# Kernel tuning notes

Measured on AMD Instinct MI355X. Metric: run time of the kernel, lower is better.

The kernel has to match this reference:

```python
import jax, jax.numpy as jnp
import numpy as np

N = 1024
X_DIM = 128
Y_DIM = 128
HID = 256


def setup_inputs() -> dict:
    key = jax.random.key(0)
    ks = jax.random.split(key, 8)
    x_samples = jax.random.normal(ks[0], (N, X_DIM), dtype=jnp.float32)
    y_samples = jax.random.normal(ks[1], (N, Y_DIM), dtype=jnp.float32)
    # F_func: Linear(x_dim+y_dim -> hidden), ReLU, Linear(hidden -> 1)
    W1 = jax.random.normal(ks[2], (HID, X_DIM + Y_DIM), dtype=jnp.float32) * 0.05
    b1 = jax.random.normal(ks[3], (HID,), dtype=jnp.float32) * 0.05
    w2 = jax.random.normal(ks[4], (HID,), dtype=jnp.float32) * 0.05  # Linear(hidden,1) weight
    b2 = jax.random.normal(ks[5], (), dtype=jnp.float32) * 0.05
    # baseline: Linear(y_dim -> 1)
    wb = jax.random.normal(ks[6], (Y_DIM,), dtype=jnp.float32) * 0.05
    bb = jax.random.normal(ks[7], (), dtype=jnp.float32) * 0.05
    return {"x_samples": x_samples, "y_samples": y_samples,
            "W1": W1, "b1": b1, "w2": w2, "b2": b2, "wb": wb, "bb": bb}


def reference(x_samples, y_samples, W1, b1, w2, b2, wb, bb):
    n = y_samples.shape[0]
    # Split first linear: F(x,y) first layer = x @ Wx^T + y @ Wy^T + b1
    # (identical math to Linear on concat([x, y]))
    Wx = W1[:, :X_DIM]  # [H, x_dim]
    Wy = W1[:, X_DIM:]  # [H, y_dim]
    px = x_samples @ Wx.T  # [N, H]
    py = y_samples @ Wy.T  # [N, H]

    # T0: F on paired samples (x_i, y_i) -> [N]
    T0 = jax.nn.relu(px + py + b1) @ w2 + b2

    # T1[i, j] = F(x_j, y_i): x tiled over dim 0, y tiled over dim 1
    h = jax.nn.relu(px[None, :, :] + py[:, None, :] + b1)  # [N, N, H]
    T1 = h @ w2 + b2  # [N, N]

    # baseline log-scores on y -> [N]
    log_scores = y_samples @ wb + bb

    # (T1 - log_scores) broadcasts log_scores along dim 1 (the j/x axis),
    # matching torch's [N,N,1] - [N,1] broadcast; logsumexp over dim 1.
    lse = jax.scipy.special.logsumexp(T1 - log_scores[None, :], axis=1)  # [N]
    log_n = jnp.log(jnp.asarray(n, dtype=T1.dtype))
    lower_bound = (1.0 + T0.mean() - log_scores.mean()
                   - jnp.exp(lse - log_n).mean())
    return lower_bound
```

## Files before the change

kernel.cpp:

```cpp
#include <hip/hip_runtime.h>
#include <hip/hip_fp16.h>

#define NN 1024
#define HID 256
#define XD 128

typedef _Float16 h2 __attribute__((ext_vector_type(2)));
typedef _Float16 h8 __attribute__((ext_vector_type(8)));

#define WSF_BYTE_OFF 1049600
#define F_C    0
#define F_PART 1024
#define F_T0P  5120
#define F_LSP  5376

__device__ __forceinline__ h2 relu2(h2 x) {
  h2 z = {(_Float16)0, (_Float16)0};
  return __builtin_elementwise_max(x, z);
}

__device__ __forceinline__ float dot2f(h2 a, h2 b, float c) {
  return __builtin_amdgcn_fdot2(a, b, c, false);
}

__global__ __launch_bounds__(256) void prep_kernel(
    const float* __restrict__ x, const float* __restrict__ y,
    const float* __restrict__ W1, const float* __restrict__ b1,
    const float* __restrict__ w2, const float* __restrict__ b2p,
    const float* __restrict__ wb, const float* __restrict__ bbp,
    _Float16* __restrict__ wsh, float* __restrict__ wsf)
{
  __shared__ float sx[4][128];
  __shared__ float sy[4][128];
  __shared__ float st0[4][4];
  __shared__ float sls[4];
  const int t = threadIdx.x;
  const int blk = blockIdx.x;
  const int r0 = blk * 4;

  {
    const int rl = (t & 127) >> 5, f = t & 31;
    if (t < 128) {
      *(float4*)&sx[rl][f * 4] = *(const float4*)(x + (r0 + rl) * XD + f * 4);
    } else {
      *(float4*)&sy[rl][f * 4] = *(const float4*)(y + (r0 + rl) * XD + f * 4);
    }
  }
  __syncthreads();

  const int k = t;
  float apx[4] = {0,0,0,0};
  float apy[4] = {0,0,0,0};
  const float* wrow = W1 + k * 256;
  for (int dq = 0; dq < 32; ++dq) {
    float4 wx = *(const float4*)(wrow + dq * 4);
    float4 wy = *(const float4*)(wrow + 128 + dq * 4);
#pragma unroll
    for (int r = 0; r < 4; ++r) {
      float4 xv = *(const float4*)&sx[r][dq * 4];
      float4 yv = *(const float4*)&sy[r][dq * 4];
      apx[r] = fmaf(xv.x, wx.x, apx[r]);
      apx[r] = fmaf(xv.y, wx.y, apx[r]);
      apx[r] = fmaf(xv.z, wx.z, apx[r]);
      apx[r] = fmaf(xv.w, wx.w, apx[r]);
      apy[r] = fmaf(yv.x, wy.x, apy[r]);
      apy[r] = fmaf(yv.y, wy.y, apy[r]);
      apy[r] = fmaf(yv.z, wy.z, apy[r]);
      apy[r] = fmaf(yv.w, wy.w, apy[r]);
    }
  }
  const float b1k = b1[k];
#pragma unroll
  for (int r = 0; r < 4; ++r) apy[r] += b1k;

  {
    _Float16* pxh = wsh;
    _Float16* pyh = wsh + 262144;
    const int kg = k >> 5, ks = (k >> 3) & 3, kl = k & 7;
#pragma unroll
    for (int r = 0; r < 4; ++r) {
      const int j = r0 + r;
      const int jt = j >> 7, jj = (j >> 6) & 1, ln = j & 63;
      pxh[((jt * 8 + kg) * 8 + ks * 2 + jj) * 512 + ln * 8 + kl]
          = (_Float16)apx[r];
      pyh[j * 256 + k] = (_Float16)apy[r];
    }
  }

  const float w2k = w2[k];
  const float b2v = b2p[0];
  const int wv = t >> 6, lane = t & 63;
#pragma unroll
  for (int r = 0; r < 4; ++r) {
    float v = fmaxf(apx[r] + apy[r], 0.f) * w2k;
    for (int o = 32; o > 0; o >>= 1) v += __shfl_down(v, o);
    if (lane == 0) st0[wv][r] = v;
  }

  if (t < 128) {
    const int rl = t >> 5, f = t & 31;
    float p = 0.f;
#pragma unroll
    for (int l = 0; l < 4; ++l) p = fmaf(sy[rl][f * 4 + l], wb[f * 4 + l], p);
    for (int m = 16; m > 0; m >>= 1) p += __shfl_xor(p, m);
    if (f == 0) {
      const float lsv = p + bbp[0];
      sls[rl] = lsv;
      wsf[F_C + r0 + rl] = __expf(b2v - lsv);
    }
  }
  __syncthreads();
  if (t == 0) {
    float t0s = 0.f, lss = 0.f;
#pragma unroll
    for (int r = 0; r < 4; ++r) {
      t0s += st0[0][r] + st0[1][r] + st0[2][r] + st0[3][r] + b2v;
      lss += sls[r];
    }
    wsf[F_T0P + blk] = t0s;
    wsf[F_LSP + blk] = lss;
  }
  if (blk == 0 && t < 128) {
    h2 wv2;
    wv2.x = (_Float16)w2[2 * t];
    wv2.y = (_Float16)w2[2 * t + 1];
    ((h2*)(wsh + 524288))[t] = wv2;
  }
}

__global__ __launch_bounds__(512) void main_kernel(
    const _Float16* __restrict__ wsh, float* __restrict__ wsf)
{
  __shared__ _Float16 spy[16 * 256];
  __shared__ _Float16 sw2[256];
  __shared__ float sComb[4][16][128];
  const int t = threadIdx.x;
  const int lane = t & 63;
  const int kg = t >> 6;
  const int blk = blockIdx.x;
  const int bj = blk & 7;
  const int i0 = (blk >> 3) * 16;

  h8 pxr[8];
  {
    const float4* gpx = (const float4*)wsh + ((bj * 8 + kg) * 8) * 64 + lane;
#pragma unroll
    for (int q = 0; q < 8; ++q) ((float4*)pxr)[q] = gpx[q * 64];
  }
  {
    const float4* gpy = (const float4*)(wsh + 262144 + (size_t)i0 * 256);
    ((float4*)spy)[t] = gpy[t];
    if (t < 32) ((float4*)sw2)[t] = ((const float4*)(wsh + 524288))[t];
  }
  __syncthreads();

  h8 w2r[4];
#pragma unroll
  for (int q = 0; q < 4; ++q) w2r[q] = ((const h8*)(sw2 + kg * 32))[q];

  float acc[16][2];
#pragma unroll
  for (int ii = 0; ii < 16; ++ii) { acc[ii][0] = 0.f; acc[ii][1] = 0.f; }

#pragma unroll
  for (int ii = 0; ii < 16; ++ii) {
    const h8* prow = (const h8*)(spy + ii * 256 + kg * 32);
#pragma unroll
    for (int ks = 0; ks < 4; ++ks) {
      h8 pv = prow[ks];
      const h2* p2 = (const h2*)&pv;
      const h2* wp = (const h2*)&w2r[ks];
#pragma unroll
      for (int jj = 0; jj < 2; ++jj) {
        const h2* x2 = (const h2*)&pxr[ks * 2 + jj];
        float s = acc[ii][jj];
        s = dot2f(relu2(x2[0] + p2[0]), wp[0], s);
        s = dot2f(relu2(x2[1] + p2[1]), wp[1], s);
        s = dot2f(relu2(x2[2] + p2[2]), wp[2], s);
        s = dot2f(relu2(x2[3] + p2[3]), wp[3], s);
        acc[ii][jj] = s;
      }
    }
  }

  if (kg >= 4) {
#pragma unroll
    for (int ii = 0; ii < 16; ++ii) {
      sComb[kg - 4][ii][lane]      = acc[ii][0];
      sComb[kg - 4][ii][lane + 64] = acc[ii][1];
    }
  }
  __syncthreads();
  if (kg < 4) {
#pragma unroll
    for (int ii = 0; ii < 16; ++ii) {
      acc[ii][0] += sComb[kg][ii][lane];
      acc[ii][1] += sComb[kg][ii][lane + 64];
    }
  }
  __syncthreads();
  if (kg == 2 || kg == 3) {
#pragma unroll
    for (int ii = 0; ii < 16; ++ii) {
      sComb[kg - 2][ii][lane]      = acc[ii][0];
      sComb[kg - 2][ii][lane + 64] = acc[ii][1];
    }
  }
  __syncthreads();
  if (kg < 2) {
#pragma unroll
    for (int ii = 0; ii < 16; ++ii) {
      acc[ii][0] += sComb[kg][ii][lane];
      acc[ii][1] += sComb[kg][ii][lane + 64];
    }
  }
  __syncthreads();
  if (kg == 1) {
#pragma unroll
    for (int ii = 0; ii < 16; ++ii) {
      sComb[0][ii][lane]      = acc[ii][0];
      sComb[0][ii][lane + 64] = acc[ii][1];
    }
  }
  __syncthreads();
  if (kg == 0) {
    const float* cbase = wsf + F_C + bj * 128;
    const float c0 = cbase[lane], c1 = cbase[64 + lane];
    float ts = 0.f;
#pragma unroll
    for (int ii = 0; ii < 16; ++ii) {
      ts += __expf(acc[ii][0] + sComb[0][ii][lane]) * c0;
      ts += __expf(acc[ii][1] + sComb[0][ii][lane + 64]) * c1;
    }
    for (int o = 32; o > 0; o >>= 1) ts += __shfl_down(ts, o);
    if (lane == 0) wsf[F_PART + blk] = ts;
  }
}

__global__ __launch_bounds__(256) void fin_kernel(
    const float* __restrict__ wsf, float* __restrict__ out)
{
  __shared__ float sr[4][3];
  const int t = threadIdx.x;
  float e = 0.f;
  if (t < 128) {
    float4 ev = ((const float4*)(wsf + F_PART))[t];
    e = (ev.x + ev.y) + (ev.z + ev.w);
  }
  float t0 = wsf[F_T0P + t];
  float ls = wsf[F_LSP + t];
  for (int o = 32; o > 0; o >>= 1) {
    e  += __shfl_down(e, o);
    t0 += __shfl_down(t0, o);
    ls += __shfl_down(ls, o);
  }
  if ((t & 63) == 0) {
    sr[t >> 6][0] = e;
    sr[t >> 6][1] = t0;
    sr[t >> 6][2] = ls;
  }
  __syncthreads();
  if (t == 0) {
    const float es  = sr[0][0] + sr[1][0] + sr[2][0] + sr[3][0];
    const float t0s = sr[0][1] + sr[1][1] + sr[2][1] + sr[3][1];
    const float lss = sr[0][2] + sr[1][2] + sr[2][2] + sr[3][2];
    out[0] = 1.0f + t0s * (1.0f / 1024.0f) - lss * (1.0f / 1024.0f)
                  - es * (1.0f / 1048576.0f);
  }
}

extern "C" void kernel_launch(void* const* d_in, const int* in_sizes, int n_in,
                              void* d_out, int out_size, void* d_ws, size_t ws_size,
                              hipStream_t stream) {
  const float* x  = (const float*)d_in[0];
  const float* y  = (const float*)d_in[1];
  const float* W1 = (const float*)d_in[2];
  const float* b1 = (const float*)d_in[3];
  const float* w2 = (const float*)d_in[4];
  const float* b2 = (const float*)d_in[5];
  const float* wb = (const float*)d_in[6];
  const float* bb = (const float*)d_in[7];
  _Float16* wsh = (_Float16*)d_ws;
  float* wsf = (float*)((char*)d_ws + WSF_BYTE_OFF);
  float* out = (float*)d_out;

  hipLaunchKernelGGL(prep_kernel, dim3(256), dim3(256), 0, stream,
                     x, y, W1, b1, w2, b2, wb, bb, wsh, wsf);
  hipLaunchKernelGGL(main_kernel, dim3(512), dim3(512), 0, stream, wsh, wsf);
  hipLaunchKernelGGL(fin_kernel, dim3(1), dim3(256), 0, stream, wsf, out);
}
```

Baseline: 35.68 us.

## Split hidden dim across blocks, write partial T1, add combine kernel

Retiles the main kernel so each block handles half the hidden dimension (kh) for 8 i-rows by 256 j-columns, doubling the grid to 1024 blocks with a launch-bounds occupancy hint. The px layout in prep is reorganised to match. Each half writes full fp32 partial T1 tiles (two 4 MB buffers) to workspace, and a new combine kernel sums the halves and applies exp and the per-column weights before reduction. This gives more parallelism and lower register pressure per block, at the cost of about 8 MB of extra global writes and reads plus one more kernel launch.

```diff
diff --git a/kernel.cpp b/kernel.cpp
--- a/kernel.cpp
+++ b/kernel.cpp
@@ -9,10 +9,12 @@
 typedef _Float16 h8 __attribute__((ext_vector_type(8)));
 
 #define WSF_BYTE_OFF 1049600
-#define F_C    0
-#define F_PART 1024
-#define F_T0P  5120
-#define F_LSP  5376
+#define F_C     0
+#define F_T0P   1024
+#define F_LSP   1280
+#define F_PART  1536
+#define F_PA    4096
+#define F_PB    1052672
 
 __device__ __forceinline__ h2 relu2(h2 x) {
   h2 z = {(_Float16)0, (_Float16)0};
@@ -76,12 +78,12 @@
   {
     _Float16* pxh = wsh;
     _Float16* pyh = wsh + 262144;
-    const int kg = k >> 5, ks = (k >> 3) & 3, kl = k & 7;
+    const int kh = k >> 7, kg = (k >> 4) & 7, ks = (k >> 3) & 1, kl = k & 7;
 #pragma unroll
     for (int r = 0; r < 4; ++r) {
       const int j = r0 + r;
-      const int jt = j >> 7, jj = (j >> 6) & 1, ln = j & 63;
-      pxh[((jt * 8 + kg) * 8 + ks * 2 + jj) * 512 + ln * 8 + kl]
+      const int jt = j >> 8, jj = (j >> 6) & 3, ln = j & 63;
+      pxh[(((((jt * 2 + kh) * 8 + kg) * 4 + jj) * 2 + ks) * 64 + ln) * 8 + kl]
           = (_Float16)apx[r];
       pyh[j * 256 + k] = (_Float16)apy[r];
     }
@@ -128,113 +130,149 @@
   }
 }
 
-__global__ __launch_bounds__(512) void main_kernel(
+__global__ __launch_bounds__(512, 4) void main_kernel(
     const _Float16* __restrict__ wsh, float* __restrict__ wsf)
 {
-  __shared__ _Float16 spy[16 * 256];
-  __shared__ _Float16 sw2[256];
-  __shared__ float sComb[4][16][128];
+  __shared__ _Float16 spy[8 * 128];
+  __shared__ _Float16 sw2[128];
+  __shared__ float sComb[4][8][256];
   const int t = threadIdx.x;
   const int lane = t & 63;
   const int kg = t >> 6;
   const int blk = blockIdx.x;
-  const int bj = blk & 7;
-  const int i0 = (blk >> 3) * 16;
-
-  h8 pxr[8];
+  const int kh = blk & 1;
+  const int ig = (blk >> 1) & 127;
+  const int jt = blk >> 8;
+
+  if (t < 128) {
+    const int row = t >> 4, col = t & 15;
+    ((float4*)spy)[t] =
+        ((const float4*)(wsh + 262144))[(ig * 8 + row) * 32 + kh * 16 + col];
+  } else if (t < 144) {
+    ((float4*)sw2)[t - 128] = ((const float4*)(wsh + 524288))[kh * 16 + (t - 128)];
+  }
+
+  h8 pxA[4], pxB[4];
   {
-    const float4* gpx = (const float4*)wsh + ((bj * 8 + kg) * 8) * 64 + lane;
-#pragma unroll
-    for (int q = 0; q < 8; ++q) ((float4*)pxr)[q] = gpx[q * 64];
-  }
-  {
-    const float4* gpy = (const float4*)(wsh + 262144 + (size_t)i0 * 256);
-    ((float4*)spy)[t] = gpy[t];
-    if (t < 32) ((float4*)sw2)[t] = ((const float4*)(wsh + 524288))[t];
-  }
-  __syncthreads();
-
-  h8 w2r[4];
-#pragma unroll
-  for (int q = 0; q < 4; ++q) w2r[q] = ((const h8*)(sw2 + kg * 32))[q];
-
-  float acc[16][2];
-#pragma unroll
-  for (int ii = 0; ii < 16; ++ii) { acc[ii][0] = 0.f; acc[ii][1] = 0.f; }
-
-#pragma unroll
-  for (int ii = 0; ii < 16; ++ii) {
-    const h8* prow = (const h8*)(spy + ii * 256 + kg * 32);
-#pragma unroll
-    for (int ks = 0; ks < 4; ++ks) {
-      h8 pv = prow[ks];
-      const h2* p2 = (const h2*)&pv;
-      const h2* wp = (const h2*)&w2r[ks];
-#pragma unroll
-      for (int jj = 0; jj < 2; ++jj) {
-        const h2* x2 = (const h2*)&pxr[ks * 2 + jj];
-        float s = acc[ii][jj];
-        s = dot2f(relu2(x2[0] + p2[0]), wp[0], s);
-        s = dot2f(relu2(x2[1] + p2[1]), wp[1], s);
-        s = dot2f(relu2(x2[2] + p2[2]), wp[2], s);
-        s = dot2f(relu2(x2[3] + p2[3]), wp[3], s);
-        acc[ii][jj] = s;
-      }
+    const float4* gpx = (const float4*)wsh;
+    const int pbase = (((jt * 2 + kh) * 8 + kg) * 4) * 2 * 64 + lane;
+#pragma unroll
+    for (int jj = 0; jj < 4; ++jj) {
+      *(float4*)&pxA[jj] = gpx[pbase + (jj * 2 + 0) * 64];
+      *(float4*)&pxB[jj] = gpx[pbase + (jj * 2 + 1) * 64];
+    }
+  }
+  __syncthreads();
+
+  const h8* wf = (const h8*)(sw2 + kg * 16);
+  h8 w0 = wf[0], w1 = wf[1];
+  const h2* wA = (const h2*)&w0;
+  const h2* wB = (const h2*)&w1;
+
+  float acc[8][4];
+#pragma unroll
+  for (int ii = 0; ii < 8; ++ii)
+#pragma unroll
+    for (int jj = 0; jj < 4; ++jj) acc[ii][jj] = 0.f;
+
+#pragma unroll
+  for (int ii = 0; ii < 8; ++ii) {
+    const h8* pf = (const h8*)(spy + ii * 128 + kg * 16);
+    h8 p0 = pf[0], p1 = pf[1];
+    const h2* pA = (const h2*)&p0;
+    const h2* pB = (const h2*)&p1;
+#pragma unroll
+    for (int jj = 0; jj < 4; ++jj) {
+      const h2* xA = (const h2*)&pxA[jj];
+      const h2* xB = (const h2*)&pxB[jj];
+      float s = acc[ii][jj];
+      s = dot2f(relu2(xA[0] + pA[0]), wA[0], s);
+      s = dot2f(relu2(xA[1] + pA[1]), wA[1], s);
+      s = dot2f(relu2(xA[2] + pA[2]), wA[2], s);
+      s = dot2f(relu2(xA[3] + pA[3]), wA[3], s);
+      s = dot2f(relu2(xB[0] + pB[0]), wB[0], s);
+      s = dot2f(relu2(xB[1] + pB[1]), wB[1], s);
+      s = dot2f(relu2(xB[2] + pB[2]), wB[2], s);
+      s = dot2f(relu2(xB[3] + pB[3]), wB[3], s);
+      acc[ii][jj] = s;
     }
   }
 
   if (kg >= 4) {
 #pragma unroll
-    for (int ii = 0; ii < 16; ++ii) {
-      sComb[kg - 4][ii][lane]      = acc[ii][0];
-      sComb[kg - 4][ii][lane + 64] = acc[ii][1];
-    }
+    for (int ii = 0; ii < 8; ++ii)
+#pragma unroll
+      for (int jj = 0; jj < 4; ++jj)
+        sComb[kg - 4][ii][jj * 64 + lane] = acc[ii][jj];
   }
   __syncthreads();
   if (kg < 4) {
 #pragma unroll
-    for (int ii = 0; ii < 16; ++ii) {
-      acc[ii][0] += sComb[kg][ii][lane];
-      acc[ii][1] += sComb[kg][ii][lane + 64];
-    }
+    for (int ii = 0; ii < 8; ++ii)
+#pragma unroll
+      for (int jj = 0; jj < 4; ++jj)
+        acc[ii][jj] += sComb[kg][ii][jj * 64 + lane];
   }
   __syncthreads();
   if (kg == 2 || kg == 3) {
 #pragma unroll
-    for (int ii = 0; ii < 16; ++ii) {
-      sComb[kg - 2][ii][lane]      = acc[ii][0];
-      sComb[kg - 2][ii][lane + 64] = acc[ii][1];
-    }
+    for (int ii = 0; ii < 8; ++ii)
+#pragma unroll
+      for (int jj = 0; jj < 4; ++jj)
+        sComb[kg - 2][ii][jj * 64 + lane] = acc[ii][jj];
   }
   __syncthreads();
   if (kg < 2) {
 #pragma unroll
-    for (int ii = 0; ii < 16; ++ii) {
-      acc[ii][0] += sComb[kg][ii][lane];
-      acc[ii][1] += sComb[kg][ii][lane + 64];
-    }
+    for (int ii = 0; ii < 8; ++ii)
+#pragma unroll
+      for (int jj = 0; jj < 4; ++jj)
+        acc[ii][jj] += sComb[kg][ii][jj * 64 + lane];
   }
   __syncthreads();
   if (kg == 1) {
 #pragma unroll
-    for (int ii = 0; ii < 16; ++ii) {
-      sComb[0][ii][lane]      = acc[ii][0];
-      sComb[0][ii][lane + 64] = acc[ii][1];
-    }
+    for (int ii = 0; ii < 8; ++ii)
+#pragma unroll
+      for (int jj = 0; jj < 4; ++jj)
+        sComb[0][ii][jj * 64 + lane] = acc[ii][jj];
   }
   __syncthreads();
   if (kg == 0) {
-    const float* cbase = wsf + F_C + bj * 128;
-    const float c0 = cbase[lane], c1 = cbase[64 + lane];
-    float ts = 0.f;
-#pragma unroll
-    for (int ii = 0; ii < 16; ++ii) {
-      ts += __expf(acc[ii][0] + sComb[0][ii][lane]) * c0;
-      ts += __expf(acc[ii][1] + sComb[0][ii][lane + 64]) * c1;
-    }
-    for (int o = 32; o > 0; o >>= 1) ts += __shfl_down(ts, o);
-    if (lane == 0) wsf[F_PART + blk] = ts;
-  }
+    float* pout = wsf + (kh ? F_PB : F_PA) + (size_t)((jt * 128 + ig) * 8) * 256;
+#pragma unroll
+    for (int ii = 0; ii < 8; ++ii)
+#pragma unroll
+      for (int jj = 0; jj < 4; ++jj)
+        pout[ii * 256 + jj * 64 + lane] =
+            acc[ii][jj] + sComb[0][ii][jj * 64 + lane];
+  }
+}
+
+__global__ __launch_bounds__(256) void combine_kernel(
+    const float* __restrict__ wsf, float* __restrict__ wsfo)
+{
+  __shared__ float sred[4];
+  const int t = threadIdx.x;
+  const int blk = blockIdx.x;
+  const float4* pA4 = (const float4*)(wsf + F_PA);
+  const float4* pB4 = (const float4*)(wsf + F_PB);
+  float ts = 0.f;
+#pragma unroll
+  for (int r = 0; r < 4; ++r) {
+    const int idx4 = blk * 1024 + r * 256 + t;
+    float4 a = pA4[idx4];
+    float4 b = pB4[idx4];
+    const int jt = idx4 >> 16;
+    float4 c4 = ((const float4*)(wsf + F_C + jt * 256))[idx4 & 63];
+    ts += __expf(a.x + b.x) * c4.x + __expf(a.y + b.y) * c4.y
+        + __expf(a.z + b.z) * c4.z + __expf(a.w + b.w) * c4.w;
+  }
+  for (int o = 32; o > 0; o >>= 1) ts += __shfl_down(ts, o);
+  if ((t & 63) == 0) sred[t >> 6] = ts;
+  __syncthreads();
+  if (t == 0)
+    wsfo[F_PART + blk] = (sred[0] + sred[1]) + (sred[2] + sred[3]);
 }
 
 __global__ __launch_bounds__(256) void fin_kernel(
@@ -242,11 +280,7 @@
 {
   __shared__ float sr[4][3];
   const int t = threadIdx.x;
-  float e = 0.f;
-  if (t < 128) {
-    float4 ev = ((const float4*)(wsf + F_PART))[t];
-    e = (ev.x + ev.y) + (ev.z + ev.w);
-  }
+  float e  = wsf[F_PART + t];
   float t0 = wsf[F_T0P + t];
   float ls = wsf[F_LSP + t];
   for (int o = 32; o > 0; o >>= 1) {
@@ -286,6 +320,7 @@
 
   hipLaunchKernelGGL(prep_kernel, dim3(256), dim3(256), 0, stream,
                      x, y, W1, b1, w2, b2, wb, bb, wsh, wsf);
-  hipLaunchKernelGGL(main_kernel, dim3(512), dim3(512), 0, stream, wsh, wsf);
+  hipLaunchKernelGGL(main_kernel, dim3(1024), dim3(512), 0, stream, wsh, wsf);
+  hipLaunchKernelGGL(combine_kernel, dim3(256), dim3(256), 0, stream, wsf, wsf);
   hipLaunchKernelGGL(fin_kernel, dim3(1), dim3(256), 0, stream, wsf, out);
 }
```

Measured after the change: 39.69 us. 1.11x slower.

## Fuse prep, main and final kernels into one cooperative kernel with grid syncs

Applied to the files above, without the earlier changes.

Merges the three launches into a single cooperative kernel of 256 blocks × 512 threads, separated by grid-wide syncs, to remove per-launch overhead and inter-kernel gaps. The prep phase now splits the x and y projections across the two halves of the block. The main phase has each block handle two 16-row i-tiles in a loop, so 256 blocks cover the former 512-block grid. The trade-offs are the cost of grid barriers, fewer blocks in the main phase (half the previous parallelism), and a dependence on all blocks being co-resident.

```diff
diff --git a/kernel.cpp b/kernel.cpp
--- a/kernel.cpp
+++ b/kernel.cpp
@@ -1,5 +1,6 @@
 #include <hip/hip_runtime.h>
 #include <hip/hip_fp16.h>
+#include <hip/hip_cooperative_groups.h>
 
 #define NN 1024
 #define HID 256
@@ -9,10 +10,10 @@
 typedef _Float16 h8 __attribute__((ext_vector_type(8)));
 
 #define WSF_BYTE_OFF 1049600
-#define F_C    0
-#define F_PART 1024
-#define F_T0P  5120
-#define F_LSP  5376
+#define F_C     0
+#define F_T0P   1024
+#define F_LSP   1280
+#define F_PART  1536
 
 __device__ __forceinline__ h2 relu2(h2 x) {
   h2 z = {(_Float16)0, (_Float16)0};
@@ -23,249 +24,281 @@
   return __builtin_amdgcn_fdot2(a, b, c, false);
 }
 
-__global__ __launch_bounds__(256) void prep_kernel(
+__global__ __launch_bounds__(512) void fused_kernel(
     const float* __restrict__ x, const float* __restrict__ y,
     const float* __restrict__ W1, const float* __restrict__ b1,
     const float* __restrict__ w2, const float* __restrict__ b2p,
     const float* __restrict__ wb, const float* __restrict__ bbp,
-    _Float16* __restrict__ wsh, float* __restrict__ wsf)
+    _Float16* __restrict__ wsh, float* __restrict__ wsf,
+    float* __restrict__ out)
 {
-  __shared__ float sx[4][128];
-  __shared__ float sy[4][128];
-  __shared__ float st0[4][4];
-  __shared__ float sls[4];
+  __shared__ __align__(16) char smem[41024];
   const int t = threadIdx.x;
   const int blk = blockIdx.x;
-  const int r0 = blk * 4;
 
   {
-    const int rl = (t & 127) >> 5, f = t & 31;
+    float* sx   = (float*)smem;
+    float* sy   = sx + 512;
+    float* spy2 = sy + 512;
+    float* st0  = spy2 + 1024;
+    float* sls  = st0 + 16;
+    const int r0 = blk * 4;
+
     if (t < 128) {
-      *(float4*)&sx[rl][f * 4] = *(const float4*)(x + (r0 + rl) * XD + f * 4);
+      const int rl = t >> 5, f = t & 31;
+      *(float4*)(sx + rl * 128 + f * 4) = *(const float4*)(x + (r0 + rl) * XD + f * 4);
+    } else if (t < 256) {
+      const int t2 = t - 128, rl = t2 >> 5, f = t2 & 31;
+      *(float4*)(sy + rl * 128 + f * 4) = *(const float4*)(y + (r0 + rl) * XD + f * 4);
+    }
+    __syncthreads();
+
+    const int side = t >> 8;
+    const int k = t & 255;
+    float ap[4] = {0.f, 0.f, 0.f, 0.f};
+    const float* wrow = W1 + k * 256 + side * 128;
+    const float* sm0 = side ? sy : sx;
+#pragma unroll 8
+    for (int dq = 0; dq < 32; ++dq) {
+      float4 wv = *(const float4*)(wrow + dq * 4);
+#pragma unroll
+      for (int r = 0; r < 4; ++r) {
+        float4 sv = *(const float4*)(sm0 + r * 128 + dq * 4);
+        ap[r] = fmaf(sv.x, wv.x, ap[r]);
+        ap[r] = fmaf(sv.y, wv.y, ap[r]);
+        ap[r] = fmaf(sv.z, wv.z, ap[r]);
+        ap[r] = fmaf(sv.w, wv.w, ap[r]);
+      }
+    }
+
+    if (side == 1) {
+      const float b1k = b1[k];
+#pragma unroll
+      for (int r = 0; r < 4; ++r) {
+        ap[r] += b1k;
+        spy2[r * 256 + k] = ap[r];
+        wsh[262144 + (r0 + r) * 256 + k] = (_Float16)ap[r];
+      }
     } else {
-      *(float4*)&sy[rl][f * 4] = *(const float4*)(y + (r0 + rl) * XD + f * 4);
+      const int kg = k >> 5, ks = (k >> 3) & 3, kl = k & 7;
+#pragma unroll
+      for (int r = 0; r < 4; ++r) {
+        const int j = r0 + r;
+        const int jt = j >> 7, jj = (j >> 6) & 1, ln = j & 63;
+        wsh[((jt * 8 + kg) * 8 + ks * 2 + jj) * 512 + ln * 8 + kl] = (_Float16)ap[r];
+      }
+    }
+    __syncthreads();
+
+    if (side == 0) {
+      const float w2k = w2[k];
+      const int wv = t >> 6, lane = t & 63;
+#pragma unroll
+      for (int r = 0; r < 4; ++r) {
+        float v = fmaxf(ap[r] + spy2[r * 256 + k], 0.f) * w2k;
+        for (int o = 32; o > 0; o >>= 1) v += __shfl_down(v, o);
+        if (lane == 0) st0[wv * 4 + r] = v;
+      }
+    } else if ((t & 255) < 128) {
+      const int t2 = t & 255, rl = t2 >> 5, f = t2 & 31;
+      float p = 0.f;
+#pragma unroll
+      for (int l = 0; l < 4; ++l) p = fmaf(sy[rl * 128 + f * 4 + l], wb[f * 4 + l], p);
+      for (int m = 16; m > 0; m >>= 1) p += __shfl_xor(p, m);
+      if (f == 0) {
+        const float lsv = p + bbp[0];
+        sls[rl] = lsv;
+        wsf[F_C + r0 + rl] = __expf(b2p[0] - lsv);
+      }
+    }
+    __syncthreads();
+
+    if (t == 0) {
+      const float b2v = b2p[0];
+      float t0s = 0.f, lss = 0.f;
+#pragma unroll
+      for (int r = 0; r < 4; ++r) {
+        t0s += st0[r] + st0[4 + r] + st0[8 + r] + st0[12 + r] + b2v;
+        lss += sls[r];
+      }
+      wsf[F_T0P + blk] = t0s;
+      wsf[F_LSP + blk] = lss;
+    }
+    if (blk == 0 && t < 128) {
+      h2 wv2;
+      wv2.x = (_Float16)w2[2 * t];
+      wv2.y = (_Float16)w2[2 * t + 1];
+      ((h2*)(wsh + 524288))[t] = wv2;
     }
   }
-  __syncthreads();
-
-  const int k = t;
-  float apx[4] = {0,0,0,0};
-  float apy[4] = {0,0,0,0};
-  const float* wrow = W1 + k * 256;
-  for (int dq = 0; dq < 32; ++dq) {
-    float4 wx = *(const float4*)(wrow + dq * 4);
-    float4 wy = *(const float4*)(wrow + 128 + dq * 4);
-#pragma unroll
-    for (int r = 0; r < 4; ++r) {
-      float4 xv = *(const float4*)&sx[r][dq * 4];
-      float4 yv = *(const float4*)&sy[r][dq * 4];
-      apx[r] = fmaf(xv.x, wx.x, apx[r]);
-      apx[r] = fmaf(xv.y, wx.y, apx[r]);
-      apx[r] = fmaf(xv.z, wx.z, apx[r]);
-      apx[r] = fmaf(xv.w, wx.w, apx[r]);
-      apy[r] = fmaf(yv.x, wy.x, apy[r]);
-      apy[r] = fmaf(yv.y, wy.y, apy[r]);
-      apy[r] = fmaf(yv.z, wy.z, apy[r]);
-      apy[r] = fmaf(yv.w, wy.w, apy[r]);
+
+  cooperative_groups::this_grid().sync();
+
+  {
+    _Float16* spy  = (_Float16*)smem;
+    float*    sCmb = (float*)(smem + 8192);
+    const int lane = t & 63;
+    const int kg = t >> 6;
+    const int bj = blk & 7;
+    const int ig = blk >> 3;
+
+    h8 pxr[8];
+    {
+      const float4* gpx = (const float4*)wsh + ((bj * 8 + kg) * 8) * 64 + lane;
+#pragma unroll
+      for (int q = 0; q < 8; ++q) ((float4*)pxr)[q] = gpx[q * 64];
+    }
+    h8 w2r[4];
+    {
+      const float4* gw2 = (const float4*)(wsh + 524288);
+#pragma unroll
+      for (int qq = 0; qq < 4; ++qq) ((float4*)w2r)[qq] = gw2[kg * 4 + qq];
+    }
+    const float cj0 = wsf[F_C + bj * 128 + lane];
+    const float cj1 = wsf[F_C + bj * 128 + 64 + lane];
+
+    float part = 0.f;
+#pragma unroll 1
+    for (int it = 0; it < 2; ++it) {
+      const int i0 = ig * 32 + it * 16;
+      __syncthreads();
+      ((float4*)spy)[t] = ((const float4*)(wsh + 262144))[i0 * 32 + t];
+      __syncthreads();
+
+      float acc[16][2];
+#pragma unroll
+      for (int ii = 0; ii < 16; ++ii) { acc[ii][0] = 0.f; acc[ii][1] = 0.f; }
+
+#pragma unroll
+      for (int ii = 0; ii < 16; ++ii) {
+        const h8* pf = (const h8*)(spy + ii * 256 + kg * 32);
+        h8 p0 = pf[0], p1 = pf[1], p2 = pf[2], p3 = pf[3];
+#pragma unroll
+        for (int jj = 0; jj < 2; ++jj) {
+          float s = acc[ii][jj];
+          {
+            const h2* pk = (const h2*)&p0; const h2* wk = (const h2*)&w2r[0];
+            const h2* xk = (const h2*)&pxr[jj];
+            s = dot2f(relu2(xk[0] + pk[0]), wk[0], s);
+            s = dot2f(relu2(xk[1] + pk[1]), wk[1], s);
+            s = dot2f(relu2(xk[2] + pk[2]), wk[2], s);
+            s = dot2f(relu2(xk[3] + pk[3]), wk[3], s);
+          }
+          {
+            const h2* pk = (const h2*)&p1; const h2* wk = (const h2*)&w2r[1];
+            const h2* xk = (const h2*)&pxr[2 + jj];
+            s = dot2f(relu2(xk[0] + pk[0]), wk[0], s);
+            s = dot2f(relu2(xk[1] + pk[1]), wk[1], s);
+            s = dot2f(relu2(xk[2] + pk[2]), wk[2], s);
+            s = dot2f(relu2(xk[3] + pk[3]), wk[3], s);
+          }
+          {
+            const h2* pk = (const h2*)&p2; const h2* wk = (const h2*)&w2r[2];
+            const h2* xk = (const h2*)&pxr[4 + jj];
+            s = dot2f(relu2(xk[0] + pk[0]), wk[0], s);
+            s = dot2f(relu2(xk[1] + pk[1]), wk[1], s);
+            s = dot2f(relu2(xk[2] + pk[2]), wk[2], s);
+            s = dot2f(relu2(xk[3] + pk[3]), wk[3], s);
+          }
+          {
+            const h2* pk = (const h2*)&p3; const h2* wk = (const h2*)&w2r[3];
+            const h2* xk = (const h2*)&pxr[6 + jj];
+            s = dot2f(relu2(xk[0] + pk[0]), wk[0], s);
+            s = dot2f(relu2(xk[1] + pk[1]), wk[1], s);
+            s = dot2f(relu2(xk[2] + pk[2]), wk[2], s);
+            s = dot2f(relu2(xk[3] + pk[3]), wk[3], s);
+          }
+          acc[ii][jj] = s;
+        }
+      }
+
+      if (kg >= 4) {
+#pragma unroll
+        for (int ii = 0; ii < 16; ++ii) {
+          sCmb[((kg - 4) * 16 + ii) * 128 + lane]      = acc[ii][0];
+          sCmb[((kg - 4) * 16 + ii) * 128 + 64 + lane] = acc[ii][1];
+        }
+      }
+      __syncthreads();
+      if (kg < 4) {
+#pragma unroll
+        for (int ii = 0; ii < 16; ++ii) {
+          acc[ii][0] += sCmb[(kg * 16 + ii) * 128 + lane];
+          acc[ii][1] += sCmb[(kg * 16 + ii) * 128 + 64 + lane];
+        }
+      }
+      __syncthreads();
+      if (kg == 2 || kg == 3) {
+#pragma unroll
+        for (int ii = 0; ii < 16; ++ii) {
+          sCmb[((kg - 2) * 16 + ii) * 128 + lane]      = acc[ii][0];
+          sCmb[((kg - 2) * 16 + ii) * 128 + 64 + lane] = acc[ii][1];
+        }
+      }
+      __syncthreads();
+      if (kg < 2) {
+#pragma unroll
+        for (int ii = 0; ii < 16; ++ii) {
+          acc[ii][0] += sCmb[(kg * 16 + ii) * 128 + lane];
+          acc[ii][1] += sCmb[(kg * 16 + ii) * 128 + 64 + lane];
+        }
+      }
+      __syncthreads();
+      if (kg == 1) {
+#pragma unroll
+        for (int ii = 0; ii < 16; ++ii) {
+          sCmb[ii * 128 + lane]      = acc[ii][0];
+          sCmb[ii * 128 + 64 + lane] = acc[ii][1];
+        }
+      }
+      __syncthreads();
+      if (kg == 0) {
+#pragma unroll
+        for (int ii = 0; ii < 16; ++ii) {
+          part += __expf(acc[ii][0] + sCmb[ii * 128 + lane]) * cj0;
+          part += __expf(acc[ii][1] + sCmb[ii * 128 + 64 + lane]) * cj1;
+        }
+      }
+    }
+    if (kg == 0) {
+      for (int o = 32; o > 0; o >>= 1) part += __shfl_down(part, o);
+      if (lane == 0) wsf[F_PART + blk] = part;
     }
   }
-  const float b1k = b1[k];
-#pragma unroll
-  for (int r = 0; r < 4; ++r) apy[r] += b1k;
-
-  {
-    _Float16* pxh = wsh;
-    _Float16* pyh = wsh + 262144;
-    const int kg = k >> 5, ks = (k >> 3) & 3, kl = k & 7;
-#pragma unroll
-    for (int r = 0; r < 4; ++r) {
-      const int j = r0 + r;
-      const int jt = j >> 7, jj = (j >> 6) & 1, ln = j & 63;
-      pxh[((jt * 8 + kg) * 8 + ks * 2 + jj) * 512 + ln * 8 + kl]
-          = (_Float16)apx[r];
-      pyh[j * 256 + k] = (_Float16)apy[r];
-    }
-  }
-
-  const float w2k = w2[k];
-  const float b2v = b2p[0];
-  const int wv = t >> 6, lane = t & 63;
-#pragma unroll
-  for (int r = 0; r < 4; ++r) {
-    float v = fmaxf(apx[r] + apy[r], 0.f) * w2k;
-    for (int o = 32; o > 0; o >>= 1) v += __shfl_down(v, o);
-    if (lane == 0) st0[wv][r] = v;
-  }
-
-  if (t < 128) {
-    const int rl = t >> 5, f = t & 31;
-    float p = 0.f;
-#pragma unroll
-    for (int l = 0; l < 4; ++l) p = fmaf(sy[rl][f * 4 + l], wb[f * 4 + l], p);
-    for (int m = 16; m > 0; m >>= 1) p += __shfl_xor(p, m);
-    if (f == 0) {
-      const float lsv = p + bbp[0];
-      sls[rl] = lsv;
-      wsf[F_C + r0 + rl] = __expf(b2v - lsv);
-    }
-  }
-  __syncthreads();
-  if (t == 0) {
-    float t0s = 0.f, lss = 0.f;
-#pragma unroll
-    for (int r = 0; r < 4; ++r) {
-      t0s += st0[0][r] + st0[1][r] + st0[2][r] + st0[3][r] + b2v;
-      lss += sls[r];
-    }
-    wsf[F_T0P + blk] = t0s;
-    wsf[F_LSP + blk] = lss;
-  }
-  if (blk == 0 && t < 128) {
-    h2 wv2;
-    wv2.x = (_Float16)w2[2 * t];
-    wv2.y = (_Float16)w2[2 * t + 1];
-    ((h2*)(wsh + 524288))[t] = wv2;
-  }
-}
-
-__global__ __launch_bounds__(512) void main_kernel(
-    const _Float16* __restrict__ wsh, float* __restrict__ wsf)
-{
-  __shared__ _Float16 spy[16 * 256];
-  __shared__ _Float16 sw2[256];
-  __shared__ float sComb[4][16][128];
-  const int t = threadIdx.x;
-  const int lane = t & 63;
-  const int kg = t >> 6;
-  const int blk = blockIdx.x;
-  const int bj = blk & 7;
-  const int i0 = (blk >> 3) * 16;
-
-  h8 pxr[8];
-  {
-    const float4* gpx = (const float4*)wsh + ((bj * 8 + kg) * 8) * 64 + lane;
-#pragma unroll
-    for (int q = 0; q < 8; ++q) ((float4*)pxr)[q] = gpx[q * 64];
-  }
-  {
-    const float4* gpy = (const float4*)(wsh + 262144 + (size_t)i0 * 256);
-    ((float4*)spy)[t] = gpy[t];
-    if (t < 32) ((float4*)sw2)[t] = ((const float4*)(wsh + 524288))[t];
-  }
-  __syncthreads();
-
-  h8 w2r[4];
-#pragma unroll
-  for (int q = 0; q < 4; ++q) w2r[q] = ((const h8*)(sw2 + kg * 32))[q];
-
-  float acc[16][2];
-#pragma unroll
-  for (int ii = 0; ii < 16; ++ii) { acc[ii][0] = 0.f; acc[ii][1] = 0.f; }
-
-#pragma unroll
-  for (int ii = 0; ii < 16; ++ii) {
-    const h8* prow = (const h8*)(spy + ii * 256 + kg * 32);
-#pragma unroll
-    for (int ks = 0; ks < 4; ++ks) {
-      h8 pv = prow[ks];
-      const h2* p2 = (const h2*)&pv;
-      const h2* wp = (const h2*)&w2r[ks];
-#pragma unroll
-      for (int jj = 0; jj < 2; ++jj) {
-        const h2* x2 = (const h2*)&pxr[ks * 2 + jj];
-        float s = acc[ii][jj];
-        s = dot2f(relu2(x2[0] + p2[0]), wp[0], s);
-        s = dot2f(relu2(x2[1] + p2[1]), wp[1], s);
-        s = dot2f(relu2(x2[2] + p2[2]), wp[2], s);
-        s = dot2f(relu2(x2[3] + p2[3]), wp[3], s);
-        acc[ii][jj] = s;
-      }
-    }
-  }
-
-  if (kg >= 4) {
-#pragma unroll
-    for (int ii = 0; ii < 16; ++ii) {
-      sComb[kg - 4][ii][lane]      = acc[ii][0];
-      sComb[kg - 4][ii][lane + 64] = acc[ii][1];
-    }
-  }
-  __syncthreads();
-  if (kg < 4) {
-#pragma unroll
-    for (int ii = 0; ii < 16; ++ii) {
-      acc[ii][0] += sComb[kg][ii][lane];
-      acc[ii][1] += sComb[kg][ii][lane + 64];
-    }
-  }
-  __syncthreads();
-  if (kg == 2 || kg == 3) {
-#pragma unroll
-    for (int ii = 0; ii < 16; ++ii) {
-      sComb[kg - 2][ii][lane]      = acc[ii][0];
-      sComb[kg - 2][ii][lane + 64] = acc[ii][1];
-    }
-  }
-  __syncthreads();
-  if (kg < 2) {
-#pragma unroll
-    for (int ii = 0; ii < 16; ++ii) {
-      acc[ii][0] += sComb[kg][ii][lane];
-      acc[ii][1] += sComb[kg][ii][lane + 64];
-    }
-  }
-  __syncthreads();
-  if (kg == 1) {
-#pragma unroll
-    for (int ii = 0; ii < 16; ++ii) {
-      sComb[0][ii][lane]      = acc[ii][0];
-      sComb[0][ii][lane + 64] = acc[ii][1];
-    }
-  }
-  __syncthreads();
-  if (kg == 0) {
-    const float* cbase = wsf + F_C + bj * 128;
-    const float c0 = cbase[lane], c1 = cbase[64 + lane];
-    float ts = 0.f;
-#pragma unroll
-    for (int ii = 0; ii < 16; ++ii) {
-      ts += __expf(acc[ii][0] + sComb[0][ii][lane]) * c0;
-      ts += __expf(acc[ii][1] + sComb[0][ii][lane + 64]) * c1;
-    }
-    for (int o = 32; o > 0; o >>= 1) ts += __shfl_down(ts, o);
-    if (lane == 0) wsf[F_PART + blk] = ts;
-  }
-}
-
-__global__ __launch_bounds__(256) void fin_kernel(
-    const float* __restrict__ wsf, float* __restrict__ out)
-{
-  __shared__ float sr[4][3];
-  const int t = threadIdx.x;
-  float e = 0.f;
-  if (t < 128) {
-    float4 ev = ((const float4*)(wsf + F_PART))[t];
-    e = (ev.x + ev.y) + (ev.z + ev.w);
-  }
-  float t0 = wsf[F_T0P + t];
-  float ls = wsf[F_LSP + t];
-  for (int o = 32; o > 0; o >>= 1) {
-    e  += __shfl_down(e, o);
-    t0 += __shfl_down(t0, o);
-    ls += __shfl_down(ls, o);
-  }
-  if ((t & 63) == 0) {
-    sr[t >> 6][0] = e;
-    sr[t >> 6][1] = t0;
-    sr[t >> 6][2] = ls;
-  }
-  __syncthreads();
-  if (t == 0) {
-    const float es  = sr[0][0] + sr[1][0] + sr[2][0] + sr[3][0];
-    const float t0s = sr[0][1] + sr[1][1] + sr[2][1] + sr[3][1];
-    const float lss = sr[0][2] + sr[1][2] + sr[2][2] + sr[3][2];
-    out[0] = 1.0f + t0s * (1.0f / 1024.0f) - lss * (1.0f / 1024.0f)
-                  - es * (1.0f / 1048576.0f);
+
+  cooperative_groups::this_grid().sync();
+
+  if (blk == 0) {
+    float* sr = (float*)smem;
+    float e = 0.f, t0v = 0.f, lsv = 0.f;
+    if (t < 256) {
+      e   = wsf[F_PART + t];
+      t0v = wsf[F_T0P + t];
+      lsv = wsf[F_LSP + t];
+    }
+    for (int o = 32; o > 0; o >>= 1) {
+      e   += __shfl_down(e, o);
+      t0v += __shfl_down(t0v, o);
+      lsv += __shfl_down(lsv, o);
+    }
+    __syncthreads();
+    if ((t & 63) == 0) {
+      sr[(t >> 6) * 3 + 0] = e;
+      sr[(t >> 6) * 3 + 1] = t0v;
+      sr[(t >> 6) * 3 + 2] = lsv;
+    }
+    __syncthreads();
+    if (t == 0) {
+      float es = 0.f, t0s = 0.f, lss = 0.f;
+#pragma unroll
+      for (int w = 0; w < 8; ++w) {
+        es  += sr[w * 3 + 0];
+        t0s += sr[w * 3 + 1];
+        lss += sr[w * 3 + 2];
+      }
+      out[0] = 1.0f + t0s * (1.0f / 1024.0f) - lss * (1.0f / 1024.0f)
+                    - es * (1.0f / 1048576.0f);
+    }
   }
 }
 
@@ -284,8 +317,9 @@
   float* wsf = (float*)((char*)d_ws + WSF_BYTE_OFF);
   float* out = (float*)d_out;
 
-  hipLaunchKernelGGL(prep_kernel, dim3(256), dim3(256), 0, stream,
-                     x, y, W1, b1, w2, b2, wb, bb, wsh, wsf);
-  hipLaunchKernelGGL(main_kernel, dim3(512), dim3(512), 0, stream, wsh, wsf);
-  hipLaunchKernelGGL(fin_kernel, dim3(1), dim3(256), 0, stream, wsf, out);
+  void* kargs[] = {(void*)&x, (void*)&y, (void*)&W1, (void*)&b1,
+                   (void*)&w2, (void*)&b2, (void*)&wb, (void*)&bb,
+                   (void*)&wsh, (void*)&wsf, (void*)&out};
+  hipLaunchCooperativeKernel((void*)fused_kernel, dim3(256), dim3(512),
+                             kargs, 0, stream);
 }
```

New measurement: 94.07 us. 2.64x slower.
